# Kernel tuning notes

Measured on AMD Instinct MI355X. Metric: run time of the kernel, lower is better.

## Reference

```python
import jax, jax.numpy as jnp
import numpy as np

B = 16384
F = 26          # num categorical fields
V = 100000      # vocab per field (equal sizes)
N = 13          # num numeric fields
D = 32          # embed_dim
HIDDEN = [256, 128, 64]


def setup_inputs() -> dict:
    key = jax.random.key(0)
    ks = jax.random.split(key, 16)
    x_cat = jax.random.randint(ks[0], (B, F), 0, V)
    x_num = jax.random.normal(ks[1], (B, N), dtype=jnp.float32)
    # first-order and second-order embedding tables (all fields stacked)
    emb0 = jax.random.normal(ks[2], (F, V), dtype=jnp.float32) * 0.01      # linear weights per cat value
    emb1 = jax.random.normal(ks[3], (F, V, D), dtype=jnp.float32) * 0.01   # latent vectors per cat value
    num_bias = jnp.zeros((N,), dtype=jnp.float32)
    num_emb = jax.random.normal(ks[4], (N, D), dtype=jnp.float32) * 0.01
    # MLP params: input_dim = (F+N)*D -> 256 -> 128 -> 64
    dims = [(F + N) * D] + HIDDEN
    params = {}
    for i in range(len(HIDDEN)):
        fan_in = dims[i]
        bound = 1.0 / np.sqrt(fan_in)
        params[f"W{i+1}"] = jax.random.uniform(ks[5 + 2 * i], (fan_in, dims[i + 1]), minval=-bound, maxval=bound, dtype=jnp.float32)
        params[f"b{i+1}"] = jax.random.uniform(ks[6 + 2 * i], (dims[i + 1],), minval=-bound, maxval=bound, dtype=jnp.float32)
    head_in = HIDDEN[-1] + 2
    hb = 1.0 / np.sqrt(head_in)
    Wc = jax.random.uniform(ks[11], (head_in, 1), minval=-hb, maxval=hb, dtype=jnp.float32)
    bc = jax.random.uniform(ks[12], (1,), minval=-hb, maxval=hb, dtype=jnp.float32)
    Wo = jax.random.uniform(ks[13], (head_in, 1), minval=-hb, maxval=hb, dtype=jnp.float32)
    bo = jax.random.uniform(ks[14], (1,), minval=-hb, maxval=hb, dtype=jnp.float32)
    return {"x_cat": x_cat, "x_num": x_num, "emb0": emb0, "emb1": emb1,
            "num_bias": num_bias, "num_emb": num_emb,
            "W1": params["W1"], "b1": params["b1"],
            "W2": params["W2"], "b2": params["b2"],
            "W3": params["W3"], "b3": params["b3"],
            "Wc": Wc, "bc": bc, "Wo": Wo, "bo": bo}


def reference(x_cat, x_num, emb0, emb1, num_bias, num_emb,
              W1, b1, W2, b2, W3, b3, Wc, bc, Wo, bo):
    f_idx = jnp.arange(F)
    # ---- first-order (linear) term ----
    linear_cat = emb0[f_idx[None, :], x_cat]                 # [B, F]
    linear_num = x_num * num_bias[None, :]                   # [B, N]
    linear_term = (linear_cat.sum(axis=1) + linear_num.sum(axis=1))[:, None]  # [B, 1]
    # ---- embeddings for FM + deep ----
    cat_e = emb1[f_idx[None, :], x_cat]                      # [B, F, D] fused gather
    num_e = x_num[:, :, None] * num_emb[None, :, :]          # [B, N, D]
    all_emb = jnp.concatenate([cat_e, num_e], axis=1)        # [B, F+N, D]
    # ---- FM second-order: 0.5 * sum((sum v)^2 - sum v^2) ----
    sum_emb = all_emb.sum(axis=1)                            # [B, D]
    square_sum = (all_emb * all_emb).sum(axis=1)             # [B, D]
    fm_second = 0.5 * (sum_emb * sum_emb - square_sum).sum(axis=1, keepdims=True)  # [B, 1]
    # ---- deep MLP (dropout = identity in eval) ----
    h = all_emb.reshape(all_emb.shape[0], -1)                # [B, (F+N)*D]
    h = jax.nn.relu(h @ W1 + b1)
    h = jax.nn.relu(h @ W2 + b2)
    h = jax.nn.relu(h @ W3 + b3)
    concat = jnp.concatenate([h, linear_term, fm_second], axis=1)  # [B, 66]
    logit1 = concat @ Wc + bc
    logit2 = concat @ Wo + bo
    return logit1, logit2
```

## Files before the change

kernel.cpp:

```cpp
#include <hip/hip_runtime.h>
#include <stdint.h>

#define B_ROWS 16384
#define NF 26
#define NV 100000
#define NN 13
#define ND 32
#define K1DIM 1248
#define H1DIM 256
#define H2DIM 128
#define H3DIM 64

typedef float f32x4 __attribute__((ext_vector_type(4)));
typedef short bf16x8 __attribute__((ext_vector_type(8)));

static __device__ __forceinline__ unsigned short f2bf(float f) {
    unsigned int u = __float_as_uint(f);
    unsigned int r = (u + 0x7fffu + ((u >> 16) & 1u)) >> 16;
    return (unsigned short)r;
}

#define S1P ((K1DIM/32)*H1DIM*32)
#define S2P ((H1DIM/32)*H2DIM*32)
#define S3P ((H2DIM/32)*H3DIM*32)

__global__ __launch_bounds__(256) void repack_weights(
    const float* __restrict__ W1, const float* __restrict__ W2, const float* __restrict__ W3,
    unsigned short* __restrict__ W1p, unsigned short* __restrict__ W2p, unsigned short* __restrict__ W3p)
{
    int tid = blockIdx.x * 256 + threadIdx.x;
    if (tid < S1P) {
        int kk = tid & 31; int n = (tid >> 5) & (H1DIM - 1); int kt = tid >> 13;
        W1p[tid] = f2bf(W1[(kt * 32 + kk) * H1DIM + n]);
    } else if (tid < S1P + S2P) {
        int t = tid - S1P;
        int kk = t & 31; int n = (t >> 5) & (H2DIM - 1); int kt = t >> 12;
        W2p[t] = f2bf(W2[(kt * 32 + kk) * H2DIM + n]);
    } else if (tid < S1P + S2P + S3P) {
        int t = tid - S1P - S2P;
        int kk = t & 31; int n = (t >> 5) & (H3DIM - 1); int kt = t >> 11;
        W3p[t] = f2bf(W3[(kt * 32 + kk) * H3DIM + n]);
    }
}

__global__ __launch_bounds__(256) void embed_fm(
    const int* __restrict__ x_cat, const float* __restrict__ x_num,
    const float* __restrict__ emb0, const float* __restrict__ emb1,
    const float* __restrict__ num_bias, const float* __restrict__ num_emb,
    unsigned short* __restrict__ Xp, float* __restrict__ lin_out, float* __restrict__ fm_out)
{
    int grp = threadIdx.x >> 5;
    int d   = threadIdx.x & 31;
    int row = blockIdx.x * 8 + grp;

    const int* xc = x_cat + row * NF;
    int   myidx = (d < NF) ? xc[d] : 0;
    float xn    = (d < NN) ? x_num[row * NN + d] : 0.f;

    float lv = 0.f;
    if (d < NF) lv = emb0[d * NV + myidx];
    if (d < NN) lv += xn * num_bias[d];

    unsigned short* xr = Xp + (size_t)row * K1DIM;
    float s = 0.f, q = 0.f;
#pragma unroll
    for (int f = 0; f < NF; ++f) {
        int idx = __shfl(myidx, f, 32);
        float e = emb1[((size_t)(f * NV + idx)) * ND + d];
        s += e; q += e * e;
        xr[f * ND + d] = f2bf(e);
    }
#pragma unroll
    for (int n = 0; n < NN; ++n) {
        float xv = __shfl(xn, n, 32);
        float e = xv * num_emb[n * ND + d];
        s += e; q += e * e;
        xr[(NF + n) * ND + d] = f2bf(e);
    }
    float val = s * s - q;
#pragma unroll
    for (int m = 16; m >= 1; m >>= 1) {
        val += __shfl_xor(val, m, 32);
        lv  += __shfl_xor(lv,  m, 32);
    }
    if (d == 0) { fm_out[row] = 0.5f * val; lin_out[row] = lv; }
}

template<int TMM, int TMN>
__global__ __launch_bounds__(256) void gemm_relu(
    const unsigned short* __restrict__ X, const unsigned short* __restrict__ Wp,
    const float* __restrict__ bias, unsigned short* __restrict__ Y,
    int M, int N, int K)
{
    int wave = blockIdx.x * 4 + (threadIdx.x >> 6);
    int lane = threadIdx.x & 63;
    int l15 = lane & 15, quad = lane >> 4;
    int nWaveN = N / (16 * TMN);
    int wm = wave / nWaveN, wn = wave % nWaveN;
    int m0 = wm * 16 * TMM, n0 = wn * 16 * TMN;

    f32x4 acc[TMM][TMN];
#pragma unroll
    for (int i = 0; i < TMM; i++)
#pragma unroll
        for (int j = 0; j < TMN; j++) acc[i][j] = (f32x4){0.f, 0.f, 0.f, 0.f};

    const unsigned short* aptr = X + (size_t)(m0 + l15) * K + quad * 8;
    const unsigned short* bptr = Wp + ((size_t)n0 + l15) * 32 + quad * 8;
    int KT = K >> 5;
    for (int kt = 0; kt < KT; ++kt) {
        bf16x8 a[TMM], b[TMN];
#pragma unroll
        for (int i = 0; i < TMM; i++)
            a[i] = *(const bf16x8*)(aptr + (size_t)i * 16 * K + kt * 32);
#pragma unroll
        for (int j = 0; j < TMN; j++)
            b[j] = *(const bf16x8*)(bptr + ((size_t)kt * N + j * 16) * 32);
#pragma unroll
        for (int i = 0; i < TMM; i++)
#pragma unroll
            for (int j = 0; j < TMN; j++)
                acc[i][j] = __builtin_amdgcn_mfma_f32_16x16x32_bf16(a[i], b[j], acc[i][j], 0, 0, 0);
    }
#pragma unroll
    for (int j = 0; j < TMN; j++) {
        int col = n0 + j * 16 + l15;
        float bv = bias[col];
#pragma unroll
        for (int i = 0; i < TMM; i++) {
            int rbase = m0 + i * 16 + quad * 4;
#pragma unroll
            for (int r = 0; r < 4; r++) {
                float v = acc[i][j][r] + bv;
                v = v > 0.f ? v : 0.f;
                Y[(size_t)(rbase + r) * N + col] = f2bf(v);
            }
        }
    }
}

__global__ __launch_bounds__(256) void gemm_head(
    const unsigned short* __restrict__ X, const unsigned short* __restrict__ Wp,
    const float* __restrict__ b3,
    const float* __restrict__ Wc, const float* __restrict__ bc,
    const float* __restrict__ Wo, const float* __restrict__ bo,
    const float* __restrict__ lin, const float* __restrict__ fm,
    float* __restrict__ out)
{
    const int K = H2DIM, N = H3DIM;
    int wave = blockIdx.x * 4 + (threadIdx.x >> 6);
    int lane = threadIdx.x & 63;
    int l15 = lane & 15, quad = lane >> 4;
    int m0 = wave * 16;

    f32x4 acc[4];
#pragma unroll
    for (int j = 0; j < 4; j++) acc[j] = (f32x4){0.f, 0.f, 0.f, 0.f};

    const unsigned short* aptr = X + (size_t)(m0 + l15) * K + quad * 8;
    const unsigned short* bptr = Wp + (size_t)l15 * 32 + quad * 8;
#pragma unroll
    for (int kt = 0; kt < 4; ++kt) {
        bf16x8 a = *(const bf16x8*)(aptr + kt * 32);
#pragma unroll
        for (int j = 0; j < 4; j++) {
            bf16x8 b = *(const bf16x8*)(bptr + (kt * N + j * 16) * 32);
            acc[j] = __builtin_amdgcn_mfma_f32_16x16x32_bf16(a, b, acc[j], 0, 0, 0);
        }
    }

    float s1r[4] = {0.f, 0.f, 0.f, 0.f};
    float s2r[4] = {0.f, 0.f, 0.f, 0.f};
#pragma unroll
    for (int j = 0; j < 4; j++) {
        int col = j * 16 + l15;
        float bv = b3[col], wc = Wc[col], wo = Wo[col];
#pragma unroll
        for (int r = 0; r < 4; r++) {
            float v = acc[j][r] + bv;
            v = v > 0.f ? v : 0.f;
            s1r[r] += v * wc;
            s2r[r] += v * wo;
        }
    }
#pragma unroll
    for (int r = 0; r < 4; r++) {
#pragma unroll
        for (int m = 8; m >= 1; m >>= 1) {
            s1r[r] += __shfl_xor(s1r[r], m, 16);
            s2r[r] += __shfl_xor(s2r[r], m, 16);
        }
    }
    if (l15 == 0) {
        float wc64 = Wc[64], wc65 = Wc[65], wo64 = Wo[64], wo65 = Wo[65];
        float bcv = bc[0], bov = bo[0];
#pragma unroll
        for (int r = 0; r < 4; r++) {
            int row = m0 + quad * 4 + r;
            float lt = lin[row], f2 = fm[row];
            out[row]          = s1r[r] + lt * wc64 + f2 * wc65 + bcv;
            out[B_ROWS + row] = s2r[r] + lt * wo64 + f2 * wo65 + bov;
        }
    }
}

#define OFF_XP   ((size_t)0)
#define OFF_W1P  ((size_t)40894464)
#define OFF_W2P  (OFF_W1P + 638976)
#define OFF_W3P  (OFF_W2P + 65536)
#define OFF_H1   (OFF_W3P + 16384)
#define OFF_H2   (OFF_H1 + 8388608)
#define OFF_LIN  (OFF_H2 + 4194304)
#define OFF_FM   (OFF_LIN + 65536)

extern "C" void kernel_launch(void* const* d_in, const int* in_sizes, int n_in,
                              void* d_out, int out_size, void* d_ws, size_t ws_size,
                              hipStream_t stream)
{
    const int*   x_cat    = (const int*)d_in[0];
    const float* x_num    = (const float*)d_in[1];
    const float* emb0     = (const float*)d_in[2];
    const float* emb1     = (const float*)d_in[3];
    const float* num_bias = (const float*)d_in[4];
    const float* num_emb  = (const float*)d_in[5];
    const float* W1 = (const float*)d_in[6];
    const float* b1 = (const float*)d_in[7];
    const float* W2 = (const float*)d_in[8];
    const float* b2 = (const float*)d_in[9];
    const float* W3 = (const float*)d_in[10];
    const float* b3 = (const float*)d_in[11];
    const float* Wc = (const float*)d_in[12];
    const float* bc = (const float*)d_in[13];
    const float* Wo = (const float*)d_in[14];
    const float* bo = (const float*)d_in[15];
    float* out = (float*)d_out;

    char* ws = (char*)d_ws;
    unsigned short* Xp  = (unsigned short*)(ws + OFF_XP);
    unsigned short* W1p = (unsigned short*)(ws + OFF_W1P);
    unsigned short* W2p = (unsigned short*)(ws + OFF_W2P);
    unsigned short* W3p = (unsigned short*)(ws + OFF_W3P);
    unsigned short* H1  = (unsigned short*)(ws + OFF_H1);
    unsigned short* H2  = (unsigned short*)(ws + OFF_H2);
    float* lin = (float*)(ws + OFF_LIN);
    float* fm  = (float*)(ws + OFF_FM);

    repack_weights<<<(S1P + S2P + S3P) / 256, 256, 0, stream>>>(W1, W2, W3, W1p, W2p, W3p);
    embed_fm<<<B_ROWS / 8, 256, 0, stream>>>(x_cat, x_num, emb0, emb1, num_bias, num_emb, Xp, lin, fm);
    gemm_relu<4, 4><<<256, 256, 0, stream>>>(Xp, W1p, b1, H1, B_ROWS, H1DIM, K1DIM);
    gemm_relu<2, 2><<<512, 256, 0, stream>>>(H1, W2p, b2, H2, B_ROWS, H2DIM, H1DIM);
    gemm_head<<<B_ROWS / 16 / 4, 256, 0, stream>>>(H2, W3p, b3, Wc, bc, Wo, bo, lin, fm, out);
}
```

Measured before the change: 451.0 us.

## Fuse layer-2 GEMM into head kernel and prefetch GEMM1 operands

The second MLP layer is merged with the third layer and the output head into one kernel. The 128-wide activation now stays in LDS per wave instead of making a round trip through global memory, and one launch is removed. The first GEMM now uses register double-buffering, loading the next k-tile before issuing MFMAs, and its tile changes from 4x4 to 4x2 with twice as many blocks. The risks are higher register pressure from prefetching and a fused kernel that may run with lower occupancy, because each wave computes the full 128-wide layer.

```diff
diff --git a/kernel.cpp b/kernel.cpp
--- a/kernel.cpp
+++ b/kernel.cpp
@@ -107,21 +107,38 @@
 
     const unsigned short* aptr = X + (size_t)(m0 + l15) * K + quad * 8;
     const unsigned short* bptr = Wp + ((size_t)n0 + l15) * 32 + quad * 8;
-    int KT = K >> 5;
-    for (int kt = 0; kt < KT; ++kt) {
-        bf16x8 a[TMM], b[TMN];
-#pragma unroll
-        for (int i = 0; i < TMM; i++)
-            a[i] = *(const bf16x8*)(aptr + (size_t)i * 16 * K + kt * 32);
-#pragma unroll
-        for (int j = 0; j < TMN; j++)
-            b[j] = *(const bf16x8*)(bptr + ((size_t)kt * N + j * 16) * 32);
+    const int KT = K >> 5;
+
+    bf16x8 a[TMM], b[TMN];
+#pragma unroll
+    for (int i = 0; i < TMM; i++) a[i] = *(const bf16x8*)(aptr + (size_t)i * 16 * K);
+#pragma unroll
+    for (int j = 0; j < TMN; j++) b[j] = *(const bf16x8*)(bptr + (size_t)j * 16 * 32);
+
+    for (int kt = 0; kt < KT - 1; ++kt) {
+        bf16x8 an[TMM], bn[TMN];
+        const unsigned short* ap = aptr + (size_t)(kt + 1) * 32;
+        const unsigned short* bp = bptr + (size_t)(kt + 1) * N * 32;
+#pragma unroll
+        for (int i = 0; i < TMM; i++) an[i] = *(const bf16x8*)(ap + (size_t)i * 16 * K);
+#pragma unroll
+        for (int j = 0; j < TMN; j++) bn[j] = *(const bf16x8*)(bp + (size_t)j * 16 * 32);
 #pragma unroll
         for (int i = 0; i < TMM; i++)
 #pragma unroll
             for (int j = 0; j < TMN; j++)
                 acc[i][j] = __builtin_amdgcn_mfma_f32_16x16x32_bf16(a[i], b[j], acc[i][j], 0, 0, 0);
-    }
+#pragma unroll
+        for (int i = 0; i < TMM; i++) a[i] = an[i];
+#pragma unroll
+        for (int j = 0; j < TMN; j++) b[j] = bn[j];
+    }
+#pragma unroll
+    for (int i = 0; i < TMM; i++)
+#pragma unroll
+        for (int j = 0; j < TMN; j++)
+            acc[i][j] = __builtin_amdgcn_mfma_f32_16x16x32_bf16(a[i], b[j], acc[i][j], 0, 0, 0);
+
 #pragma unroll
     for (int j = 0; j < TMN; j++) {
         int col = n0 + j * 16 + l15;
@@ -139,33 +156,64 @@
     }
 }
 
-__global__ __launch_bounds__(256) void gemm_head(
-    const unsigned short* __restrict__ X, const unsigned short* __restrict__ Wp,
-    const float* __restrict__ b3,
+#define LDP 136
+__global__ __launch_bounds__(256) void gemm23_head(
+    const unsigned short* __restrict__ H1, const unsigned short* __restrict__ W2p,
+    const float* __restrict__ b2,
+    const unsigned short* __restrict__ W3p, const float* __restrict__ b3,
     const float* __restrict__ Wc, const float* __restrict__ bc,
     const float* __restrict__ Wo, const float* __restrict__ bo,
     const float* __restrict__ lin, const float* __restrict__ fm,
     float* __restrict__ out)
 {
-    const int K = H2DIM, N = H3DIM;
-    int wave = blockIdx.x * 4 + (threadIdx.x >> 6);
+    __shared__ unsigned short lds[4 * 16 * LDP];
+    int wid  = threadIdx.x >> 6;
+    int wave = blockIdx.x * 4 + wid;
     int lane = threadIdx.x & 63;
     int l15 = lane & 15, quad = lane >> 4;
     int m0 = wave * 16;
-
-    f32x4 acc[4];
-#pragma unroll
-    for (int j = 0; j < 4; j++) acc[j] = (f32x4){0.f, 0.f, 0.f, 0.f};
-
-    const unsigned short* aptr = X + (size_t)(m0 + l15) * K + quad * 8;
-    const unsigned short* bptr = Wp + (size_t)l15 * 32 + quad * 8;
+    unsigned short* wlds = lds + wid * 16 * LDP;
+
+    f32x4 acc2[8];
+#pragma unroll
+    for (int j = 0; j < 8; j++) acc2[j] = (f32x4){0.f, 0.f, 0.f, 0.f};
+
+    const unsigned short* aptr = H1 + (size_t)(m0 + l15) * H1DIM + quad * 8;
+    const unsigned short* bptr = W2p + l15 * 32 + quad * 8;
+#pragma unroll
+    for (int kt = 0; kt < 8; ++kt) {
+        bf16x8 a = *(const bf16x8*)(aptr + kt * 32);
+#pragma unroll
+        for (int j = 0; j < 8; j++) {
+            bf16x8 b = *(const bf16x8*)(bptr + (kt * H2DIM + j * 16) * 32);
+            acc2[j] = __builtin_amdgcn_mfma_f32_16x16x32_bf16(a, b, acc2[j], 0, 0, 0);
+        }
+    }
+#pragma unroll
+    for (int j = 0; j < 8; j++) {
+        int col = j * 16 + l15;
+        float bv = b2[col];
+#pragma unroll
+        for (int r = 0; r < 4; r++) {
+            float v = acc2[j][r] + bv;
+            v = v > 0.f ? v : 0.f;
+            wlds[(quad * 4 + r) * LDP + col] = f2bf(v);
+        }
+    }
+    __syncthreads();
+
+    f32x4 acc3[4];
+#pragma unroll
+    for (int j = 0; j < 4; j++) acc3[j] = (f32x4){0.f, 0.f, 0.f, 0.f};
+
+    const unsigned short* b3ptr = W3p + l15 * 32 + quad * 8;
 #pragma unroll
     for (int kt = 0; kt < 4; ++kt) {
-        bf16x8 a = *(const bf16x8*)(aptr + kt * 32);
+        bf16x8 a = *(const bf16x8*)(wlds + l15 * LDP + kt * 32 + quad * 8);
 #pragma unroll
         for (int j = 0; j < 4; j++) {
-            bf16x8 b = *(const bf16x8*)(bptr + (kt * N + j * 16) * 32);
-            acc[j] = __builtin_amdgcn_mfma_f32_16x16x32_bf16(a, b, acc[j], 0, 0, 0);
+            bf16x8 b = *(const bf16x8*)(b3ptr + (kt * H3DIM + j * 16) * 32);
+            acc3[j] = __builtin_amdgcn_mfma_f32_16x16x32_bf16(a, b, acc3[j], 0, 0, 0);
         }
     }
 
@@ -177,7 +225,7 @@
         float bv = b3[col], wc = Wc[col], wo = Wo[col];
 #pragma unroll
         for (int r = 0; r < 4; r++) {
-            float v = acc[j][r] + bv;
+            float v = acc3[j][r] + bv;
             v = v > 0.f ? v : 0.f;
             s1r[r] += v * wc;
             s2r[r] += v * wo;
@@ -209,8 +257,7 @@
 #define OFF_W2P  (OFF_W1P + 638976)
 #define OFF_W3P  (OFF_W2P + 65536)
 #define OFF_H1   (OFF_W3P + 16384)
-#define OFF_H2   (OFF_H1 + 8388608)
-#define OFF_LIN  (OFF_H2 + 4194304)
+#define OFF_LIN  (OFF_H1 + 8388608)
 #define OFF_FM   (OFF_LIN + 65536)
 
 extern "C" void kernel_launch(void* const* d_in, const int* in_sizes, int n_in,
@@ -241,13 +288,11 @@
     unsigned short* W2p = (unsigned short*)(ws + OFF_W2P);
     unsigned short* W3p = (unsigned short*)(ws + OFF_W3P);
     unsigned short* H1  = (unsigned short*)(ws + OFF_H1);
-    unsigned short* H2  = (unsigned short*)(ws + OFF_H2);
     float* lin = (float*)(ws + OFF_LIN);
     float* fm  = (float*)(ws + OFF_FM);
 
     repack_weights<<<(S1P + S2P + S3P) / 256, 256, 0, stream>>>(W1, W2, W3, W1p, W2p, W3p);
     embed_fm<<<B_ROWS / 8, 256, 0, stream>>>(x_cat, x_num, emb0, emb1, num_bias, num_emb, Xp, lin, fm);
-    gemm_relu<4, 4><<<256, 256, 0, stream>>>(Xp, W1p, b1, H1, B_ROWS, H1DIM, K1DIM);
-    gemm_relu<2, 2><<<512, 256, 0, stream>>>(H1, W2p, b2, H2, B_ROWS, H2DIM, H1DIM);
-    gemm_head<<<B_ROWS / 16 / 4, 256, 0, stream>>>(H2, W3p, b3, Wc, bc, Wo, bo, lin, fm, out);
-}
+    gemm_relu<4, 2><<<512, 256, 0, stream>>>(Xp, W1p, b1, H1, B_ROWS, H1DIM, K1DIM);
+    gemm23_head<<<B_ROWS / 16 / 4, 256, 0, stream>>>(H1, W2p, b2, W3p, b3, Wc, bc, Wo, bo, lin, fm, out);
+}
```

After: 458.5 us. About the same (+1.7%).
